# Kernel tuning notes

Measured on AMD Instinct MI355X. Metric: run time of the kernel, lower is better.

The kernel has to match this reference:

```python
import jax, jax.numpy as jnp
from jax import lax
import numpy as np

B, NW, L, E, H, V = 8192, 4, 16, 128, 128, 64  # batch, words/example, max chars, emsize, hidden, char vocab


def setup_inputs() -> dict:
    key = jax.random.key(0)
    ks = jax.random.split(key, 13)
    s = 0.05
    return {
        "word_ids": jax.random.randint(ks[0], (B, NW, L), 0, V, dtype=jnp.int32),
        "lengths": jax.random.randint(ks[1], (B, NW), 1, L + 1, dtype=jnp.int32),
        "emb_i": jax.random.normal(ks[2], (V, E), jnp.float32),
        "W_ih": jax.random.normal(ks[3], (4 * H, E), jnp.float32) * s,
        "W_hh": jax.random.normal(ks[4], (4 * H, H), jnp.float32) * s,
        "b_ih": jax.random.normal(ks[5], (4 * H,), jnp.float32) * s,
        "b_hh": jax.random.normal(ks[6], (4 * H,), jnp.float32) * s,
        "conv1_w": jax.random.normal(ks[7], (4, 1, 2, 2), jnp.float32) * 0.5,
        "conv1_b": jax.random.normal(ks[8], (4,), jnp.float32) * 0.1,
        "conv2_w": jax.random.normal(ks[9], (8, 4, 2, 2), jnp.float32) * 0.5,
        "conv2_b": jax.random.normal(ks[10], (8,), jnp.float32) * 0.1,
        "scorer_w": jax.random.normal(ks[11], (1, 2 * 2 * 8), jnp.float32) * 0.2,
        "scorer_b": jax.random.normal(ks[12], (1,), jnp.float32) * 0.1,
    }


def reference(word_ids, lengths, emb_i, W_ih, W_hh, b_ih, b_hh,
              conv1_w, conv1_b, conv2_w, conv2_b, scorer_w, scorer_b):
    Bx, NWx, Lx = word_ids.shape
    Hh = W_hh.shape[1]
    BN = Bx * NWx
    # char embeddings for all words, packed: [L, BN, E]
    xs = emb_i[word_ids.reshape(BN, Lx)].transpose(1, 0, 2)
    # ragged lengths -> per-step update mask [L, BN]
    mask = jnp.arange(Lx, dtype=lengths.dtype)[:, None] < lengths.reshape(-1)[None, :]
    h0 = jnp.zeros((BN, Hh), emb_i.dtype)

    def step(carry, xm):
        h, c = carry
        x_t, m = xm
        gates = x_t @ W_ih.T + b_ih + h @ W_hh.T + b_hh  # torch LSTMCell gate order i,f,g,o
        i, f, g, o = jnp.split(gates, 4, axis=-1)
        i = jax.nn.sigmoid(i); f = jax.nn.sigmoid(f)
        g = jnp.tanh(g); o = jax.nn.sigmoid(o)
        c_new = f * c + i * g
        h_new = o * jnp.tanh(c_new)
        m = m[:, None]
        return (jnp.where(m, h_new, h), jnp.where(m, c_new, c)), None

    (h, c), _ = lax.scan(step, (h0, h0), (xs, mask))
    # Model.encode returns the cell state c
    reps = c.reshape(Bx, NWx, Hh)

    # pairwise cosine similarity matrix [B, NW, NW]
    norms = jnp.sqrt(jnp.sum(reps * reps, axis=-1))
    dots = jnp.einsum('bih,bjh->bij', reps, reps)
    cos = dots / (norms[:, :, None] * norms[:, None, :])

    # tiny 2-layer CNN scorer on the NWxNW matrix (NCHW)
    dn = ('NCHW', 'OIHW', 'NCHW')
    x_img = cos[:, None, :, :]
    out = jax.nn.relu(lax.conv_general_dilated(x_img, conv1_w, (1, 1), 'VALID', dimension_numbers=dn)
                      + conv1_b[None, :, None, None])
    out = jax.nn.relu(lax.conv_general_dilated(out, conv2_w, (1, 1), 'VALID', dimension_numbers=dn)
                      + conv2_b[None, :, None, None])
    flat = out.reshape(Bx, -1)  # channel-major flatten matches torch .view
    score = flat @ scorer_w.T + scorer_b
    return jax.nn.sigmoid(score)  # [B, 1] discriminator prob
```

## Files before the change

kernel.cpp:

```cpp
#include <hip/hip_runtime.h>

#define BSZ    8192
#define NWRD   4
#define SEQL   16
#define HDIM   128
#define NSEQ   (BSZ * NWRD)
#define WGSEQ  32
#define UPB    80
#define BINCAP (UPB * WGSEQ)
#define NUNITS (16 * UPB)
#define HSTRIDE 136

typedef float  f32x4  __attribute__((ext_vector_type(4)));
typedef float  f32x16 __attribute__((ext_vector_type(16)));
typedef __bf16 bf16x8 __attribute__((ext_vector_type(8)));

union AccU { f32x16 v; f32x4 q[4]; float f[16]; };
union HPack { unsigned short s[4]; unsigned long long u64; };

__device__ __forceinline__ unsigned short f2bf(float f) {
    unsigned int u = __builtin_bit_cast(unsigned int, f);
    return (unsigned short)((u + 0x7fff + ((u >> 16) & 1)) >> 16);
}
__device__ __forceinline__ float sigm(float x) {
    return __builtin_amdgcn_rcpf(1.f + __builtin_amdgcn_exp2f(x * -1.44269504f));
}
__device__ __forceinline__ float tanhx(float x) {
    return 1.f - 2.f * __builtin_amdgcn_rcpf(1.f + __builtin_amdgcn_exp2f(x * 2.88539008f));
}

__global__ void prep4(const float* __restrict__ emb, const float* __restrict__ W_ih,
                      const float* __restrict__ b_ih, const float* __restrict__ b_hh,
                      const float* __restrict__ W_hh, const int* __restrict__ lengths,
                      float* __restrict__ P2T, unsigned short* __restrict__ WA,
                      int* __restrict__ perm, int* __restrict__ gh)
{
    __shared__ int lh[16], gbase[16];
    const int blk = blockIdx.x, tid = threadIdx.x;

    if (blk < 128) {
        int idx = blk * 256 + tid;
        int v = idx >> 9, g = (idx >> 7) & 3, j = idx & 127;
        int n = g * 128 + j;
        float s = b_ih[n] + b_hh[n];
        const float* er = emb  + v * 128;
        const float* wr = W_ih + n * 128;
        for (int e = 0; e < 128; e += 4)
            s += er[e]*wr[e] + er[e+1]*wr[e+1] + er[e+2]*wr[e+2] + er[e+3]*wr[e+3];
        P2T[idx] = s;
    } else if (blk < 384) {
        int idx = (blk - 128) * 256 + tid;
        int jj = idx & 7, lane = (idx >> 3) & 63, kc = (idx >> 9) & 7, tt = idx >> 12;
        int wv = tt >> 2, g = tt & 3;
        int n = g * 128 + wv * 32 + (lane & 31);
        int k = kc * 16 + (lane >> 5) * 8 + jj;
        WA[idx] = f2bf(W_hh[n * 128 + k]);
    } else {
        if (tid < 16) lh[tid] = 0;
        __syncthreads();
        int i = (blk - 384) * 256 + tid;
        int b = 16 - lengths[i];
        int rank = atomicAdd(&lh[b], 1);
        __syncthreads();
        if (tid < 16) gbase[tid] = atomicAdd(&gh[tid], lh[tid]);
        __syncthreads();
        perm[b * BINCAP + gbase[b] + rank] = i;
    }
}

__global__ __launch_bounds__(256, 2) void lstm4(
    const int* __restrict__ word_ids, const int* __restrict__ perm,
    const int* __restrict__ gh, const float* __restrict__ P2T,
    const unsigned short* __restrict__ WA, float* __restrict__ c_out)
{
    __shared__ __align__(16) unsigned short hbuf[2][WGSEQ * HSTRIDE];
    __shared__ int words_s[WGSEQ * 17];
    __shared__ int sid_s[WGSEQ];

    const int tid    = threadIdx.x;
    const int wv     = tid >> 6;
    const int lane   = tid & 63;
    const int lane31 = lane & 31;
    const int hl     = lane >> 5;

    const int u    = blockIdx.x;
    const int b    = u / UPB;
    const int widx = u % UPB;
    const int cnt  = gh[b];
    const int ml   = (widx * WGSEQ < cnt) ? (16 - b) : 0;

    bf16x8 afr[4][8];
#pragma unroll
    for (int g = 0; g < 4; ++g)
#pragma unroll
        for (int kc = 0; kc < 8; ++kc)
            afr[g][kc] = *(const bf16x8*)(WA + (((wv * 4 + g) * 8 + kc) * 64 + lane) * 8);

    if (tid < WGSEQ) {
        int slot = widx * WGSEQ + tid;
        sid_s[tid] = (slot < cnt) ? perm[b * BINCAP + slot] : 0;
    }
    for (int i = tid; i < WGSEQ * HSTRIDE; i += 256) ((int*)hbuf)[i] = 0;
    __syncthreads();
    for (int i = tid; i < WGSEQ * SEQL; i += 256)
        words_s[(i >> 4) * 17 + (i & 15)] = word_ids[sid_s[i >> 4] * SEQL + (i & 15)];
    __syncthreads();

    if (ml > 0) {
        f32x4 cq[4] = {{0,0,0,0},{0,0,0,0},{0,0,0,0},{0,0,0,0}};
        const char* P2c  = (const char*)P2T;
        const int pboff  = wv * 128 + hl * 16;
        const int rdo    = lane31 * HSTRIDE;
        const int jbase  = wv * 32 + 4 * hl;

#pragma unroll 1
        for (int t = 0; t < ml; ++t) {
            const unsigned short* __restrict__ hr = hbuf[t & 1];
            unsigned short*       __restrict__ hw = hbuf[(t + 1) & 1];

            const int w = words_s[lane31 * 17 + t];
            const char* pb = P2c + ((size_t)w << 11) + pboff;
            AccU acc[4];
#pragma unroll
            for (int g = 0; g < 4; ++g)
#pragma unroll
                for (int q = 0; q < 4; ++q)
                    acc[g].q[q] = *(const f32x4*)(pb + g * 512 + q * 32);

            bf16x8 bf[8];
#pragma unroll
            for (int kc = 0; kc < 8; ++kc)
                bf[kc] = *(const bf16x8*)(hr + rdo + kc * 16 + hl * 8);

#pragma unroll
            for (int kc = 0; kc < 8; ++kc) {
                const bf16x8 bb = bf[kc];
#pragma unroll
                for (int g = 0; g < 4; ++g)
                    acc[g].v = __builtin_amdgcn_mfma_f32_32x32x16_bf16(afr[g][kc], bb, acc[g].v, 0, 0, 0);
            }

#pragma unroll
            for (int q = 0; q < 4; ++q) {
                HPack hp;
#pragma unroll
                for (int d = 0; d < 4; ++d) {
                    const int r = q * 4 + d;
                    float ig = sigm(acc[0].f[r]);
                    float fg = sigm(acc[1].f[r]);
                    float gg = tanhx(acc[2].f[r]);
                    float og = sigm(acc[3].f[r]);
                    float cn = fg * cq[q][d] + ig * gg;
                    cq[q][d] = cn;
                    hp.s[d] = f2bf(og * tanhx(cn));
                }
                *(unsigned long long*)(hw + rdo + jbase + 8 * q) = hp.u64;
            }
            __syncthreads();
        }

        if (widx * WGSEQ + lane31 < cnt) {
            const int sid = sid_s[lane31];
#pragma unroll
            for (int q = 0; q < 4; ++q)
                *(f32x4*)(c_out + sid * HDIM + jbase + 8 * q) = cq[q];
        }
    }
}

__global__ __launch_bounds__(256) void epilogue(
    const float* __restrict__ c_ws,
    const float* __restrict__ conv1_w, const float* __restrict__ conv1_b,
    const float* __restrict__ conv2_w, const float* __restrict__ conv2_b,
    const float* __restrict__ scorer_w, const float* __restrict__ scorer_b,
    float* __restrict__ out)
{
    __shared__ __align__(16) float reps[8 * NWRD * HDIM];
    __shared__ float gram_s[8 * 16];

    const int tid = threadIdx.x;
    const int b0  = blockIdx.x * 8;

    for (int i = tid; i < 8 * NWRD * HDIM; i += 256)
        reps[i] = c_ws[b0 * NWRD * HDIM + i];
    __syncthreads();

    const int bt  = tid >> 5;
    const int sub = tid & 31;

    float dval = 0.f;
    if (sub < 16) {
        int i = sub >> 2, j = sub & 3;
        const f32x4* ci = (const f32x4*)(reps + (bt * 4 + i) * HDIM);
        const f32x4* cj = (const f32x4*)(reps + (bt * 4 + j) * HDIM);
        f32x4 s4 = {0.f, 0.f, 0.f, 0.f};
        for (int k = 0; k < HDIM / 4; ++k) s4 += ci[k] * cj[k];
        dval = s4.x + s4.y + s4.z + s4.w;
        gram_s[bt * 16 + sub] = dval;
    }
    __syncthreads();
    float cosv = 0.f;
    if (sub < 16) {
        int i = sub >> 2, j = sub & 3;
        float di = gram_s[bt * 16 + i * 4 + i];
        float dj = gram_s[bt * 16 + j * 4 + j];
        cosv = __fdividef(dval, sqrtf(di * dj));
    }
    __syncthreads();
    if (sub < 16) gram_s[bt * 16 + sub] = cosv;
    __syncthreads();

    if (sub == 0) {
        float img[4][4];
#pragma unroll
        for (int i = 0; i < 4; ++i)
#pragma unroll
            for (int j = 0; j < 4; ++j) img[i][j] = gram_s[bt * 16 + i * 4 + j];

        float o1[4][3][3];
#pragma unroll
        for (int ch = 0; ch < 4; ++ch) {
            float w00 = conv1_w[ch*4+0], w01 = conv1_w[ch*4+1];
            float w10 = conv1_w[ch*4+2], w11 = conv1_w[ch*4+3];
            float bb  = conv1_b[ch];
#pragma unroll
            for (int y = 0; y < 3; ++y)
#pragma unroll
                for (int x = 0; x < 3; ++x) {
                    float s = bb + w00*img[y][x]   + w01*img[y][x+1]
                                 + w10*img[y+1][x] + w11*img[y+1][x+1];
                    o1[ch][y][x] = s > 0.f ? s : 0.f;
                }
        }
        float sc = scorer_b[0];
#pragma unroll
        for (int oc = 0; oc < 8; ++oc) {
            float bb = conv2_b[oc];
#pragma unroll
            for (int y = 0; y < 2; ++y)
#pragma unroll
                for (int x = 0; x < 2; ++x) {
                    float s = bb;
#pragma unroll
                    for (int ic = 0; ic < 4; ++ic) {
                        const float* w = conv2_w + oc * 16 + ic * 4;
                        s += w[0]*o1[ic][y][x]   + w[1]*o1[ic][y][x+1]
                           + w[2]*o1[ic][y+1][x] + w[3]*o1[ic][y+1][x+1];
                    }
                    float rl = s > 0.f ? s : 0.f;
                    sc += rl * scorer_w[oc * 4 + y * 2 + x];
                }
        }
        out[blockIdx.x * 8 + bt] = sigm(sc);
    }
}

extern "C" void kernel_launch(void* const* d_in, const int* in_sizes, int n_in,
                              void* d_out, int out_size, void* d_ws, size_t ws_size,
                              hipStream_t stream)
{
    const int*   word_ids = (const int*)d_in[0];
    const int*   lengths  = (const int*)d_in[1];
    const float* emb      = (const float*)d_in[2];
    const float* W_ih     = (const float*)d_in[3];
    const float* W_hh     = (const float*)d_in[4];
    const float* b_ih     = (const float*)d_in[5];
    const float* b_hh     = (const float*)d_in[6];
    const float* conv1_w  = (const float*)d_in[7];
    const float* conv1_b  = (const float*)d_in[8];
    const float* conv2_w  = (const float*)d_in[9];
    const float* conv2_b  = (const float*)d_in[10];
    const float* scorer_w = (const float*)d_in[11];
    const float* scorer_b = (const float*)d_in[12];
    float* out = (float*)d_out;

    char* ws = (char*)d_ws;
    float*          P2T  = (float*)(ws + 0);
    unsigned short* WA   = (unsigned short*)(ws + (128<<10));
    int*            perm = (int*)(ws + (256<<10));
    int*            gh   = (int*)(ws + (416<<10));
    float*          c_ws = (float*)(ws + (512<<10));

    hipMemsetAsync(gh, 0, 16 * sizeof(int), stream);
    prep4   <<<512,   256, 0, stream>>>(emb, W_ih, b_ih, b_hh, W_hh, lengths,
                                        P2T, WA, perm, gh);
    lstm4   <<<NUNITS, 256, 0, stream>>>(word_ids, perm, gh, P2T, WA, c_ws);
    epilogue<<<BSZ / 8, 256, 0, stream>>>(c_ws, conv1_w, conv1_b, conv2_w, conv2_b,
                                          scorer_w, scorer_b, out);
}
```

Before: 197.6 us.

## Pack LSTM workgroups densely across length bins and prefetch next-step input projections

Measured after the change: 250.5 us. +26.7%, slower.

```diff
diff --git a/kernel.cpp b/kernel.cpp
--- a/kernel.cpp
+++ b/kernel.cpp
@@ -8,7 +8,7 @@
 #define WGSEQ  32
 #define UPB    80
 #define BINCAP (UPB * WGSEQ)
-#define NUNITS (16 * UPB)
+#define NUNITS 1040
 #define HSTRIDE 136
 
 typedef float  f32x4  __attribute__((ext_vector_type(4)));
@@ -68,7 +68,7 @@
     }
 }
 
-__global__ __launch_bounds__(256, 2) void lstm4(
+__global__ __launch_bounds__(256, 2) void lstm5(
     const int* __restrict__ word_ids, const int* __restrict__ perm,
     const int* __restrict__ gh, const float* __restrict__ P2T,
     const unsigned short* __restrict__ WA, float* __restrict__ c_out)
@@ -83,11 +83,19 @@
     const int lane31 = lane & 31;
     const int hl     = lane >> 5;
 
-    const int u    = blockIdx.x;
-    const int b    = u / UPB;
-    const int widx = u % UPB;
-    const int cnt  = gh[b];
-    const int ml   = (widx * WGSEQ < cnt) ? (16 - b) : 0;
+    const int u = blockIdx.x;
+    int b = -1, grp = 0, cnt = 0;
+    {
+        int acc0 = 0;
+        for (int bb = 0; bb < 16; ++bb) {
+            int c  = gh[bb];
+            int ng = (c + 31) >> 5;
+            if (u < acc0 + ng) { b = bb; grp = u - acc0; cnt = c; break; }
+            acc0 += ng;
+        }
+    }
+    if (b < 0) return;
+    const int L = 16 - b;
 
     bf16x8 afr[4][8];
 #pragma unroll
@@ -97,8 +105,8 @@
             afr[g][kc] = *(const bf16x8*)(WA + (((wv * 4 + g) * 8 + kc) * 64 + lane) * 8);
 
     if (tid < WGSEQ) {
-        int slot = widx * WGSEQ + tid;
-        sid_s[tid] = (slot < cnt) ? perm[b * BINCAP + slot] : 0;
+        int slot = grp * WGSEQ + tid;
+        sid_s[tid] = perm[b * BINCAP + (slot < cnt ? slot : 0)];
     }
     for (int i = tid; i < WGSEQ * HSTRIDE; i += 256) ((int*)hbuf)[i] = 0;
     __syncthreads();
@@ -106,65 +114,80 @@
         words_s[(i >> 4) * 17 + (i & 15)] = word_ids[sid_s[i >> 4] * SEQL + (i & 15)];
     __syncthreads();
 
-    if (ml > 0) {
-        f32x4 cq[4] = {{0,0,0,0},{0,0,0,0},{0,0,0,0},{0,0,0,0}};
-        const char* P2c  = (const char*)P2T;
-        const int pboff  = wv * 128 + hl * 16;
-        const int rdo    = lane31 * HSTRIDE;
-        const int jbase  = wv * 32 + 4 * hl;
+    f32x4 cq[4] = {{0,0,0,0},{0,0,0,0},{0,0,0,0},{0,0,0,0}};
+    const char* P2c  = (const char*)P2T;
+    const int pboff  = wv * 128 + hl * 16;
+    const int rdo    = lane31 * HSTRIDE;
+    const int jbase  = wv * 32 + 4 * hl;
+
+    f32x4 pf[4][4];
+    {
+        const char* pb = P2c + ((size_t)words_s[lane31 * 17] << 11) + pboff;
+#pragma unroll
+        for (int g = 0; g < 4; ++g)
+#pragma unroll
+            for (int q = 0; q < 4; ++q)
+                pf[g][q] = *(const f32x4*)(pb + g * 512 + q * 32);
+    }
 
 #pragma unroll 1
-        for (int t = 0; t < ml; ++t) {
-            const unsigned short* __restrict__ hr = hbuf[t & 1];
-            unsigned short*       __restrict__ hw = hbuf[(t + 1) & 1];
-
-            const int w = words_s[lane31 * 17 + t];
-            const char* pb = P2c + ((size_t)w << 11) + pboff;
-            AccU acc[4];
+    for (int t = 0; t < L; ++t) {
+        const unsigned short* __restrict__ hr = hbuf[t & 1];
+        unsigned short*       __restrict__ hw = hbuf[(t + 1) & 1];
+
+        AccU acc[4];
+#pragma unroll
+        for (int g = 0; g < 4; ++g)
+#pragma unroll
+            for (int q = 0; q < 4; ++q)
+                acc[g].q[q] = pf[g][q];
+
+        if (t + 1 < L) {
+            const char* pb = P2c + ((size_t)words_s[lane31 * 17 + t + 1] << 11) + pboff;
 #pragma unroll
             for (int g = 0; g < 4; ++g)
 #pragma unroll
                 for (int q = 0; q < 4; ++q)
-                    acc[g].q[q] = *(const f32x4*)(pb + g * 512 + q * 32);
-
-            bf16x8 bf[8];
-#pragma unroll
-            for (int kc = 0; kc < 8; ++kc)
-                bf[kc] = *(const bf16x8*)(hr + rdo + kc * 16 + hl * 8);
-
-#pragma unroll
-            for (int kc = 0; kc < 8; ++kc) {
-                const bf16x8 bb = bf[kc];
-#pragma unroll
-                for (int g = 0; g < 4; ++g)
-                    acc[g].v = __builtin_amdgcn_mfma_f32_32x32x16_bf16(afr[g][kc], bb, acc[g].v, 0, 0, 0);
+                    pf[g][q] = *(const f32x4*)(pb + g * 512 + q * 32);
+        }
+
+        bf16x8 bf[8];
+#pragma unroll
+        for (int kc = 0; kc < 8; ++kc)
+            bf[kc] = *(const bf16x8*)(hr + rdo + kc * 16 + hl * 8);
+
+#pragma unroll
+        for (int kc = 0; kc < 8; ++kc) {
+            const bf16x8 bb = bf[kc];
+#pragma unroll
+            for (int g = 0; g < 4; ++g)
+                acc[g].v = __builtin_amdgcn_mfma_f32_32x32x16_bf16(afr[g][kc], bb, acc[g].v, 0, 0, 0);
+        }
+
+#pragma unroll
+        for (int q = 0; q < 4; ++q) {
+            HPack hp;
+#pragma unroll
+            for (int d = 0; d < 4; ++d) {
+                const int r = q * 4 + d;
+                float ig = sigm(acc[0].f[r]);
+                float fg = sigm(acc[1].f[r]);
+                float gg = tanhx(acc[2].f[r]);
+                float og = sigm(acc[3].f[r]);
+                float cn = fg * cq[q][d] + ig * gg;
+                cq[q][d] = cn;
+                hp.s[d] = f2bf(og * tanhx(cn));
             }
-
-#pragma unroll
-            for (int q = 0; q < 4; ++q) {
-                HPack hp;
-#pragma unroll
-                for (int d = 0; d < 4; ++d) {
-                    const int r = q * 4 + d;
-                    float ig = sigm(acc[0].f[r]);
-                    float fg = sigm(acc[1].f[r]);
-                    float gg = tanhx(acc[2].f[r]);
-                    float og = sigm(acc[3].f[r]);
-                    float cn = fg * cq[q][d] + ig * gg;
-                    cq[q][d] = cn;
-                    hp.s[d] = f2bf(og * tanhx(cn));
-                }
-                *(unsigned long long*)(hw + rdo + jbase + 8 * q) = hp.u64;
-            }
-            __syncthreads();
-        }
-
-        if (widx * WGSEQ + lane31 < cnt) {
-            const int sid = sid_s[lane31];
-#pragma unroll
-            for (int q = 0; q < 4; ++q)
-                *(f32x4*)(c_out + sid * HDIM + jbase + 8 * q) = cq[q];
-        }
+            *(unsigned long long*)(hw + rdo + jbase + 8 * q) = hp.u64;
+        }
+        __syncthreads();
+    }
+
+    if (grp * WGSEQ + lane31 < cnt) {
+        const int sid = sid_s[lane31];
+#pragma unroll
+        for (int q = 0; q < 4; ++q)
+            *(f32x4*)(c_out + sid * HDIM + jbase + 8 * q) = cq[q];
     }
 }
 
@@ -278,13 +301,13 @@
     float*          P2T  = (float*)(ws + 0);
     unsigned short* WA   = (unsigned short*)(ws + (128<<10));
     int*            perm = (int*)(ws + (256<<10));
-    int*            gh   = (int*)(ws + (416<<10));
+    int*            gh   = (int*)(ws + (424<<10));
     float*          c_ws = (float*)(ws + (512<<10));
 
     hipMemsetAsync(gh, 0, 16 * sizeof(int), stream);
-    prep4   <<<512,   256, 0, stream>>>(emb, W_ih, b_ih, b_hh, W_hh, lengths,
-                                        P2T, WA, perm, gh);
-    lstm4   <<<NUNITS, 256, 0, stream>>>(word_ids, perm, gh, P2T, WA, c_ws);
+    prep4   <<<512,    256, 0, stream>>>(emb, W_ih, b_ih, b_hh, W_hh, lengths,
+                                         P2T, WA, perm, gh);
+    lstm5   <<<NUNITS, 256, 0, stream>>>(word_ids, perm, gh, P2T, WA, c_ws);
     epilogue<<<BSZ / 8, 256, 0, stream>>>(c_ws, conv1_w, conv1_b, conv2_w, conv2_b,
                                           scorer_w, scorer_b, out);
 }
```
